# Kernel optimization log

Measured on AMD Instinct MI355X. Metric: run time of the kernel, lower is better.

The kernel has to match this reference:

```python
import jax, jax.numpy as jnp
import numpy as np

LN_EPS = 1e-5

def setup_inputs() -> dict:
    key = jax.random.key(0)
    ks = jax.random.split(key, 8)
    B, L, D, H = 4, 2048, 512, 8
    x = jax.random.normal(ks[0], (B, L, D), dtype=jnp.float32)
    token_ids = jax.random.randint(ks[1], (B, L), 0, 50000, dtype=jnp.int64)
    s = 1.0 / np.sqrt(D)
    Wq = jax.random.normal(ks[2], (D, D), dtype=jnp.float32) * s
    Wk = jax.random.normal(ks[3], (D, D), dtype=jnp.float32) * s
    Wv = jax.random.normal(ks[4], (D, D), dtype=jnp.float32) * s
    Wo = jax.random.normal(ks[5], (D, D), dtype=jnp.float32) * s
    gamma = jnp.ones((D,), dtype=jnp.float32)
    beta = jnp.zeros((D,), dtype=jnp.float32)
    return {"x": x, "token_ids": token_ids, "Wq": Wq, "Wk": Wk,
            "Wv": Wv, "Wo": Wo, "gamma": gamma, "beta": beta}

def reference(x, token_ids, Wq, Wk, Wv, Wo, gamma, beta):
    B, L, D = x.shape
    H = 8
    Dh = D // H
    residual = x
    # Pre-LN
    mu = jnp.mean(x, axis=-1, keepdims=True)
    var = jnp.mean(jnp.square(x - mu), axis=-1, keepdims=True)
    xn = (x - mu) * jax.lax.rsqrt(var + LN_EPS) * gamma + beta
    # projections (torch Linear: y = x @ W.T), split heads -> [B,H,L,Dh]
    def proj(W):
        return jnp.einsum('bld,ed->ble', xn, W).reshape(B, L, H, Dh).transpose(0, 2, 1, 3)
    Q, K, V = proj(Wq), proj(Wk), proj(Wv)
    scale = jnp.sqrt(jnp.float32(Dh))
    scores = jnp.einsum('bhqd,bhkd->bhqk', Q, K) / scale  # [B,H,L,L]
    neg_inf = jnp.float32(-jnp.inf)
    causal = jnp.triu(jnp.ones((L, L), dtype=bool), k=1)           # [L,L]
    pad = (token_ids == 0)[:, None, None, :]                       # [B,1,1,L]
    scores = jnp.where(causal[None, None], neg_inf, scores)
    scores = jnp.where(pad, neg_inf, scores)
    all_masked = jnp.all(jnp.isinf(scores), axis=-1, keepdims=True)
    scores = jnp.where(all_masked, 0.0, scores)
    attn = jax.nn.softmax(scores, axis=-1)  # dropout is identity in eval
    out = jnp.einsum('bhqk,bhkd->bhqd', attn, V)
    out = out.transpose(0, 2, 1, 3).reshape(B, L, D)
    out = jnp.einsum('bld,ed->ble', out, Wo)
    return residual + out
```

## Files before the change

kernel.cpp:

```cpp
#include <hip/hip_runtime.h>
#include <math.h>

typedef unsigned short u16;
typedef unsigned int u32;
typedef unsigned long long u64;
typedef float f32x4 __attribute__((ext_vector_type(4)));
typedef __bf16 bf16x8 __attribute__((ext_vector_type(8)));
typedef __bf16 bf16x4 __attribute__((ext_vector_type(4)));

constexpr int Bc = 4, Lc = 2048, Dc = 512, Hc = 8, DHc = 64;
constexpr int NTOK = Bc * Lc;
constexpr float LN_EPS = 1e-5f;
constexpr int PS = 72;
constexpr float QSCALE = 0.125f * 1.44269504088896340736f;
constexpr float MNEG = -1e30f;

__device__ inline u16 bf_bits(float f) {
  return __builtin_bit_cast(u16, (__bf16)f);
}

__global__ __launch_bounds__(256) void prep2_kernel(const float* __restrict__ s0,
                                                    const float* __restrict__ s1,
                                                    const float* __restrict__ s2,
                                                    const float* __restrict__ s3,
                                                    u16* __restrict__ d0,
                                                    u16* __restrict__ d1,
                                                    u16* __restrict__ d2,
                                                    u16* __restrict__ d3,
                                                    const int* __restrict__ tok,
                                                    u64* __restrict__ pm,
                                                    float* __restrict__ vm,
                                                    const float* __restrict__ x,
                                                    const float* __restrict__ gamma,
                                                    const float* __restrict__ beta,
                                                    u16* __restrict__ xn) {
  int bid = blockIdx.x;
  if (bid < 1024) {
    int mat = bid >> 8;
    int i = ((bid & 255) * 256 + threadIdx.x) * 4;
    const float* s = (mat == 0) ? s0 : (mat == 1) ? s1 : (mat == 2) ? s2 : s3;
    u16* d = (mat == 0) ? d0 : (mat == 1) ? d1 : (mat == 2) ? d2 : d3;
    float4 v = *(const float4*)&s[i];
    bf16x4 o;
    o[0] = (__bf16)v.x; o[1] = (__bf16)v.y; o[2] = (__bf16)v.z; o[3] = (__bf16)v.w;
    *(bf16x4*)&d[i] = o;
  } else if (bid < 1056) {
    int wid = ((bid - 1024) * 256 + threadIdx.x) >> 6;
    int lane = threadIdx.x & 63;
    u64 m = __ballot(tok[(size_t)wid * 64 + lane] == 0);
    if (lane == 0) pm[wid] = m;
    if (bid == 1024) {
      float4 z = make_float4(0.f, 0.f, 0.f, 0.f);
      *(float4*)&vm[threadIdx.x * 8] = z;
      *(float4*)&vm[threadIdx.x * 8 + 4] = z;
    }
  } else {
    int wave = threadIdx.x >> 6;
    int lane = threadIdx.x & 63;
    int row  = (bid - 1056) * 4 + wave;
    const float* xr = x + (size_t)row * Dc;
    float4 v0 = ((const float4*)xr)[lane * 2];
    float4 v1 = ((const float4*)xr)[lane * 2 + 1];
    float sum = v0.x + v0.y + v0.z + v0.w + v1.x + v1.y + v1.z + v1.w;
    float sq  = v0.x*v0.x + v0.y*v0.y + v0.z*v0.z + v0.w*v0.w
              + v1.x*v1.x + v1.y*v1.y + v1.z*v1.z + v1.w*v1.w;
    #pragma unroll
    for (int off = 32; off > 0; off >>= 1) {
      sum += __shfl_xor(sum, off);
      sq  += __shfl_xor(sq, off);
    }
    float mu = sum * (1.0f / Dc);
    float rs = rsqrtf(sq * (1.0f / Dc) - mu * mu + LN_EPS);
    float4 g0 = ((const float4*)gamma)[lane * 2];
    float4 g1 = ((const float4*)gamma)[lane * 2 + 1];
    float4 b0 = ((const float4*)beta)[lane * 2];
    float4 b1 = ((const float4*)beta)[lane * 2 + 1];
    bf16x8 o;
    o[0] = (__bf16)((v0.x - mu) * rs * g0.x + b0.x);
    o[1] = (__bf16)((v0.y - mu) * rs * g0.y + b0.y);
    o[2] = (__bf16)((v0.z - mu) * rs * g0.z + b0.z);
    o[3] = (__bf16)((v0.w - mu) * rs * g0.w + b0.w);
    o[4] = (__bf16)((v1.x - mu) * rs * g1.x + b1.x);
    o[5] = (__bf16)((v1.y - mu) * rs * g1.y + b1.y);
    o[6] = (__bf16)((v1.z - mu) * rs * g1.z + b1.z);
    o[7] = (__bf16)((v1.w - mu) * rs * g1.w + b1.w);
    *(bf16x8*)&xn[(size_t)row * Dc + lane * 8] = o;
  }
}

template <int MODE>
__global__ __launch_bounds__(256) void gemm_bf16(const u16* __restrict__ A,
                                                 const u16* __restrict__ W,
                                                 const float* __restrict__ res,
                                                 float* __restrict__ out_f,
                                                 u16* __restrict__ o_q,
                                                 u16* __restrict__ o_k,
                                                 u16* __restrict__ o_v,
                                                 float* __restrict__ vm) {
  __shared__ u16 As[2][128 * 64];
  __shared__ u16 Bs[2][128 * 64];
  int tid = threadIdx.x;
  int lane = tid & 63;
  int w = tid >> 6;
  int wr = w >> 1, wc = w & 1;
  int cc = lane & 15, rb = lane >> 4;
  int n0 = blockIdx.x * 128;
  int e0 = blockIdx.y * 128;

  auto stage = [&](int k0, int buf) {
    #pragma unroll
    for (int i = 0; i < 4; i++) {
      int s = (i * 4 + w) * 64 + lane;
      int row = s >> 3;
      int colp = (s & 7) ^ (row & 7);
      const char* gA = (const char*)&A[(size_t)(n0 + row) * Dc + k0] + colp * 16;
      const char* gB = (const char*)&W[(size_t)(e0 + row) * Dc + k0] + colp * 16;
      __builtin_amdgcn_global_load_lds(
          (const __attribute__((address_space(1))) void*)gA,
          (__attribute__((address_space(3))) void*)&As[buf][(i * 4 + w) * 512], 16, 0, 0);
      __builtin_amdgcn_global_load_lds(
          (const __attribute__((address_space(1))) void*)gB,
          (__attribute__((address_space(3))) void*)&Bs[buf][(i * 4 + w) * 512], 16, 0, 0);
    }
  };

  f32x4 acc[4][4] = {};
  stage(0, 0);
  for (int kt = 0; kt < 8; kt++) {
    int cur = kt & 1;
    if (kt < 7) {
      stage((kt + 1) << 6, cur ^ 1);
      asm volatile("s_waitcnt vmcnt(8)" ::: "memory");
    } else {
      asm volatile("s_waitcnt vmcnt(0)" ::: "memory");
    }
    __builtin_amdgcn_sched_barrier(0);
    __builtin_amdgcn_s_barrier();
    __builtin_amdgcn_sched_barrier(0);
    #pragma unroll
    for (int kk = 0; kk < 2; kk++) {
      bf16x8 aF[4], bF[4];
      #pragma unroll
      for (int m = 0; m < 4; m++) {
        int row = wr * 64 + m * 16 + cc;
        int cp = ((rb + kk * 4) ^ (cc & 7)) << 3;
        aF[m] = *(bf16x8*)&As[cur][row * 64 + cp];
      }
      #pragma unroll
      for (int n = 0; n < 4; n++) {
        int row = wc * 64 + n * 16 + cc;
        int cp = ((rb + kk * 4) ^ (cc & 7)) << 3;
        bF[n] = *(bf16x8*)&Bs[cur][row * 64 + cp];
      }
      #pragma unroll
      for (int m = 0; m < 4; m++)
        #pragma unroll
        for (int n = 0; n < 4; n++)
          acc[m][n] = __builtin_amdgcn_mfma_f32_16x16x32_bf16(aF[m], bF[n], acc[m][n], 0, 0, 0);
    }
    __syncthreads();
  }

  if (MODE == 3) {
    int bb = n0 >> 11;
    int mat = e0 >> 9;
    int e0c = e0 & 511;
    if (mat == 2) {
      #pragma unroll
      for (int n = 0; n < 4; n++) {
        int c = e0c + wc * 64 + n * 16 + cc;
        int h = c >> 6, dh = c & 63;
        float cp = 0.f;
        #pragma unroll
        for (int m = 0; m < 4; m++) {
          int l = (n0 + wr * 64 + m * 16 + rb * 4) & (Lc - 1);
          bf16x4 o4;
          o4[0] = (__bf16)acc[m][n][0]; o4[1] = (__bf16)acc[m][n][1];
          o4[2] = (__bf16)acc[m][n][2]; o4[3] = (__bf16)acc[m][n][3];
          size_t addr = ((((size_t)(bb * Hc + h)) * (Lc / 64) + (l >> 6)) * DHc + dh) * 64 + (l & 63);
          *(bf16x4*)&o_v[addr] = o4;
          cp += (acc[m][n][0] + acc[m][n][1]) + (acc[m][n][2] + acc[m][n][3]);
        }
        cp += __shfl_xor(cp, 16);
        cp += __shfl_xor(cp, 32);
        if (lane < 16) atomicAdd(&vm[(bb * Hc + h) * DHc + dh], cp);
      }
    } else {
      float sc = (mat == 0) ? QSCALE : 1.0f;
      u16* dst = (mat == 0) ? o_q : o_k;
      #pragma unroll
      for (int m = 0; m < 4; m++) {
        #pragma unroll
        for (int n = 0; n < 4; n++) {
          #pragma unroll
          for (int j = 0; j < 4; j++) {
            int r = n0 + wr * 64 + m * 16 + rb * 4 + j;
            int c = e0c + wc * 64 + n * 16 + cc;
            int ll = r & (Lc - 1);
            dst[(((size_t)(bb * Hc + (c >> 6))) * Lc + ll) * DHc + (c & 63)] = bf_bits(acc[m][n][j] * sc);
          }
        }
      }
    }
  } else {
    #pragma unroll
    for (int m = 0; m < 4; m++) {
      #pragma unroll
      for (int n = 0; n < 4; n++) {
        #pragma unroll
        for (int j = 0; j < 4; j++) {
          int r = n0 + wr * 64 + m * 16 + rb * 4 + j;
          int c = e0 + wc * 64 + n * 16 + cc;
          size_t o = (size_t)r * Dc + c;
          out_f[o] = acc[m][n][j] + res[o];
        }
      }
    }
  }
}

__global__ __launch_bounds__(64) void attn11(const u16* __restrict__ Q,
                                             const u16* __restrict__ K,
                                             const u16* __restrict__ VT,
                                             const float* __restrict__ vm,
                                             const u64* __restrict__ pmask,
                                             u16* __restrict__ out) {
  __shared__ u16 Ps[32 * PS];
  int lane = threadIdx.x;
  int cc = lane & 15, rb = lane >> 4;
  int bh = blockIdx.x;
  int qt = (int)gridDim.y - 1 - (int)blockIdx.y;
  int q0 = qt * 32;
  int b = bh >> 3, h = bh & 7;
  const u16* Qb = Q + (size_t)bh * Lc * DHc;
  const u16* Kb = K + (size_t)bh * Lc * DHc;
  const u16* Vb = VT + (size_t)bh * Lc * DHc;
  const u64* pmb = pmask + (b << 5);
  int nfull = q0 >> 6;

  bf16x8 qF[2][2];
  #pragma unroll
  for (int qb = 0; qb < 2; qb++)
    #pragma unroll
    for (int kc = 0; kc < 2; kc++)
      qF[qb][kc] = *(const bf16x8*)&Qb[(size_t)(q0 + qb * 16 + cc) * DHc + kc * 32 + rb * 8];

  float mrow[2] = {MNEG, MNEG};
  float lrow[2] = {0.f, 0.f};
  f32x4 acc[2][4] = {};

  bf16x8 kfA[4][2], kfB[4][2];
  {
    const u16* kp = Kb;
    #pragma unroll
    for (int c = 0; c < 4; c++) {
      kfA[c][0] = *(const bf16x8*)&kp[(c * 16 + cc) * DHc + rb * 8];
      kfA[c][1] = *(const bf16x8*)&kp[(c * 16 + cc) * DHc + 32 + rb * 8];
    }
  }
  if (nfull >= 1) {
    const u16* kp = Kb + (size_t)64 * DHc;
    #pragma unroll
    for (int c = 0; c < 4; c++) {
      kfB[c][0] = *(const bf16x8*)&kp[(c * 16 + cc) * DHc + rb * 8];
      kfB[c][1] = *(const bf16x8*)&kp[(c * 16 + cc) * DHc + 32 + rb * 8];
    }
  }

  auto body = [&](int kt, bf16x8 (&kf)[4][2]) {
    int k0 = kt * 64;
    bool last = (kt == nfull);
    u64 pm = pmb[kt];
    const u16* vp = Vb + (size_t)kt * (DHc * 64);
    bf16x8 vf[2][4];
    #pragma unroll
    for (int kc = 0; kc < 2; kc++)
      #pragma unroll
      for (int d0 = 0; d0 < 4; d0++)
        vf[kc][d0] = *(const bf16x8*)&vp[(d0 * 16 + cc) * 64 + kc * 32 + rb * 8];

    f32x4 sq[2][4] = {};
    __builtin_amdgcn_s_setprio(1);
    #pragma unroll
    for (int c = 0; c < 4; c++) {
      #pragma unroll
      for (int qb = 0; qb < 2; qb++) {
        sq[qb][c] = __builtin_amdgcn_mfma_f32_16x16x32_bf16(kf[c][0], qF[qb][0], sq[qb][c], 0, 0, 0);
        sq[qb][c] = __builtin_amdgcn_mfma_f32_16x16x32_bf16(kf[c][1], qF[qb][1], sq[qb][c], 0, 0, 0);
      }
    }
    __builtin_amdgcn_s_setprio(0);
    if (kt + 2 <= nfull) {
      const u16* kp = Kb + (size_t)(k0 + 128) * DHc;
      #pragma unroll
      for (int c = 0; c < 4; c++) {
        kf[c][0] = *(const bf16x8*)&kp[(c * 16 + cc) * DHc + rb * 8];
        kf[c][1] = *(const bf16x8*)&kp[(c * 16 + cc) * DHc + 32 + rb * 8];
      }
    }
    if (pm) {
      #pragma unroll
      for (int c = 0; c < 4; c++) {
        u32 smr = (((u32)(pm >> (c * 16)) & 0xffffu) >> (rb * 4));
        #pragma unroll
        for (int qb = 0; qb < 2; qb++)
          #pragma unroll
          for (int j = 0; j < 4; j++)
            if ((smr >> j) & 1) sq[qb][c][j] = -INFINITY;
      }
    }
    if (last) {
      #pragma unroll
      for (int qb = 0; qb < 2; qb++) {
        int qrel = q0 + qb * 16 + cc - k0;
        #pragma unroll
        for (int c = 0; c < 4; c++)
          #pragma unroll
          for (int j = 0; j < 4; j++)
            if (c * 16 + rb * 4 + j > qrel) sq[qb][c][j] = -INFINITY;
      }
    }
    #pragma unroll
    for (int qb = 0; qb < 2; qb++) {
      float m0 = fmaxf(fmaxf(sq[qb][0][0], sq[qb][0][1]), fmaxf(sq[qb][0][2], sq[qb][0][3]));
      float m1 = fmaxf(fmaxf(sq[qb][1][0], sq[qb][1][1]), fmaxf(sq[qb][1][2], sq[qb][1][3]));
      float m2 = fmaxf(fmaxf(sq[qb][2][0], sq[qb][2][1]), fmaxf(sq[qb][2][2], sq[qb][2][3]));
      float m3 = fmaxf(fmaxf(sq[qb][3][0], sq[qb][3][1]), fmaxf(sq[qb][3][2], sq[qb][3][3]));
      float mx = fmaxf(fmaxf(m0, m1), fmaxf(m2, m3));
      mx = fmaxf(mx, __shfl_xor(mx, 16));
      mx = fmaxf(mx, __shfl_xor(mx, 32));
      if (!__all(mx <= mrow[qb] + 8.f)) {
        float nm = fmaxf(mrow[qb], mx);
        float alpha = exp2f(mrow[qb] - nm);
        lrow[qb] *= alpha;
        #pragma unroll
        for (int d0 = 0; d0 < 4; d0++)
          #pragma unroll
          for (int j = 0; j < 4; j++)
            acc[qb][d0][j] *= alpha;
        mrow[qb] = nm;
      }
      float rs = 0.f;
      #pragma unroll
      for (int c = 0; c < 4; c++) {
        f32x4 p;
        #pragma unroll
        for (int j = 0; j < 4; j++) p[j] = exp2f(sq[qb][c][j] - mrow[qb]);
        rs += (p[0] + p[1]) + (p[2] + p[3]);
        bf16x4 p4;
        p4[0] = (__bf16)p[0]; p4[1] = (__bf16)p[1];
        p4[2] = (__bf16)p[2]; p4[3] = (__bf16)p[3];
        *(bf16x4*)&Ps[(qb * 16 + cc) * PS + c * 16 + rb * 4] = p4;
      }
      rs += __shfl_xor(rs, 16);
      rs += __shfl_xor(rs, 32);
      lrow[qb] += rs;
    }
    asm volatile("s_waitcnt lgkmcnt(0)" ::: "memory");
    __builtin_amdgcn_sched_barrier(0);
    __builtin_amdgcn_s_setprio(1);
    #pragma unroll
    for (int kc = 0; kc < 2; kc++) {
      bf16x8 pF0 = *(bf16x8*)&Ps[(size_t)cc * PS + kc * 32 + rb * 8];
      bf16x8 pF1 = *(bf16x8*)&Ps[(size_t)(16 + cc) * PS + kc * 32 + rb * 8];
      #pragma unroll
      for (int d0 = 0; d0 < 4; d0++) {
        acc[0][d0] = __builtin_amdgcn_mfma_f32_16x16x32_bf16(vf[kc][d0], pF0, acc[0][d0], 0, 0, 0);
        acc[1][d0] = __builtin_amdgcn_mfma_f32_16x16x32_bf16(vf[kc][d0], pF1, acc[1][d0], 0, 0, 0);
      }
    }
    __builtin_amdgcn_s_setprio(0);
  };

  for (int kt = 0; kt <= nfull; kt += 2) {
    body(kt, kfA);
    if (kt + 1 <= nfull) body(kt + 1, kfB);
  }

  #pragma unroll
  for (int qb = 0; qb < 2; qb++) {
    int q = q0 + qb * 16 + cc;
    bool ok = lrow[qb] > 0.f;
    float inv = ok ? 1.0f / lrow[qb] : 0.f;
    #pragma unroll
    for (int d0 = 0; d0 < 4; d0++) {
      bf16x4 o4;
      #pragma unroll
      for (int j = 0; j < 4; j++) {
        float v = ok ? acc[qb][d0][j] * inv
                     : vm[bh * DHc + d0 * 16 + rb * 4 + j] * (1.0f / Lc);
        o4[j] = (__bf16)v;
      }
      *(bf16x4*)&out[((size_t)(b * Lc + q)) * Dc + h * DHc + d0 * 16 + rb * 4] = o4;
    }
  }
}

extern "C" void kernel_launch(void* const* d_in, const int* in_sizes, int n_in,
                              void* d_out, int out_size, void* d_ws, size_t ws_size,
                              hipStream_t stream) {
  const float* x     = (const float*)d_in[0];
  const int*   tok   = (const int*)d_in[1];
  const float* Wq    = (const float*)d_in[2];
  const float* Wk    = (const float*)d_in[3];
  const float* Wv    = (const float*)d_in[4];
  const float* Wo    = (const float*)d_in[5];
  const float* gamma = (const float*)d_in[6];
  const float* beta  = (const float*)d_in[7];
  float* out = (float*)d_out;

  const size_t SEG = (size_t)NTOK * Dc;
  const size_t WSEG = (size_t)Dc * Dc;
  u16* xn   = (u16*)d_ws;
  u16* Qd   = xn + SEG;
  u16* Kd   = Qd + SEG;
  u16* VT   = Kd + SEG;
  u16* ao   = VT + SEG;
  u16* Wqkv = ao + SEG;
  u16* Wob  = Wqkv + 3 * WSEG;
  float* vm = (float*)(Wob + WSEG);
  u64* pmarr = (u64*)(vm + (size_t)Bc * Hc * DHc);

  prep2_kernel<<<3104, 256, 0, stream>>>(Wq, Wk, Wv, Wo,
                                         Wqkv, Wqkv + WSEG, Wqkv + 2 * WSEG, Wob,
                                         tok, pmarr, vm, x, gamma, beta, xn);

  dim3 gq(NTOK / 128, (3 * Dc) / 128);
  gemm_bf16<3><<<gq, 256, 0, stream>>>(xn, Wqkv, nullptr, nullptr, Qd, Kd, VT, vm);

  dim3 ga(Bc * Hc, Lc / 32);
  attn11<<<ga, 64, 0, stream>>>(Qd, Kd, VT, vm, pmarr, ao);

  dim3 gg(NTOK / 128, Dc / 128);
  gemm_bf16<0><<<gg, 256, 0, stream>>>(ao, Wob, x, out, nullptr, nullptr, nullptr, nullptr);
}
```

Measured before the change: 106.5 us.

## Rewrite attention with 32x32x16 MFMA and register-resident P via lane shuffles

The attention kernel now uses 32x32x16 bf16 MFMA tiles, with one 32-query row per lane pair, in place of 16x16x32 tiles. The softmax probabilities are packed to bf16 and exchanged across half-waves with shuffles to form the PV operand directly, so the LDS round trip for P is gone. The K double-buffer prefetch is dropped, and K is now loaded each iteration right before use. Output is staged through LDS so each lane writes 16-byte stores. This risks exposed K load latency, and the shuffle-based P layout is intricate to get right.

```diff
diff --git a/kernel.cpp b/kernel.cpp
--- a/kernel.cpp
+++ b/kernel.cpp
@@ -5,8 +5,11 @@
 typedef unsigned int u32;
 typedef unsigned long long u64;
 typedef float f32x4 __attribute__((ext_vector_type(4)));
+typedef float f32x16 __attribute__((ext_vector_type(16)));
 typedef __bf16 bf16x8 __attribute__((ext_vector_type(8)));
 typedef __bf16 bf16x4 __attribute__((ext_vector_type(4)));
+typedef __bf16 bf16x2 __attribute__((ext_vector_type(2)));
+typedef u32 u32x4 __attribute__((ext_vector_type(4)));
 
 constexpr int Bc = 4, Lc = 2048, Dc = 512, Hc = 8, DHc = 64;
 constexpr int NTOK = Bc * Lc;
@@ -17,6 +20,10 @@
 
 __device__ inline u16 bf_bits(float f) {
   return __builtin_bit_cast(u16, (__bf16)f);
+}
+__device__ inline u32 pk2(float a, float b) {
+  bf16x2 t; t[0] = (__bf16)a; t[1] = (__bf16)b;
+  return __builtin_bit_cast(u32, t);
 }
 
 __global__ __launch_bounds__(256) void prep2_kernel(const float* __restrict__ s0,
@@ -219,7 +226,7 @@
   }
 }
 
-__global__ __launch_bounds__(64) void attn11(const u16* __restrict__ Q,
+__global__ __launch_bounds__(64) void attn12(const u16* __restrict__ Q,
                                              const u16* __restrict__ K,
                                              const u16* __restrict__ VT,
                                              const float* __restrict__ vm,
@@ -227,7 +234,8 @@
                                              u16* __restrict__ out) {
   __shared__ u16 Ps[32 * PS];
   int lane = threadIdx.x;
-  int cc = lane & 15, rb = lane >> 4;
+  int ql = lane & 31;
+  int hi = lane >> 5;
   int bh = blockIdx.x;
   int qt = (int)gridDim.y - 1 - (int)blockIdx.y;
   int q0 = qt * 32;
@@ -238,160 +246,156 @@
   const u64* pmb = pmask + (b << 5);
   int nfull = q0 >> 6;
 
-  bf16x8 qF[2][2];
+  bf16x8 qF[4];
   #pragma unroll
-  for (int qb = 0; qb < 2; qb++)
-    #pragma unroll
-    for (int kc = 0; kc < 2; kc++)
-      qF[qb][kc] = *(const bf16x8*)&Qb[(size_t)(q0 + qb * 16 + cc) * DHc + kc * 32 + rb * 8];
-
-  float mrow[2] = {MNEG, MNEG};
-  float lrow[2] = {0.f, 0.f};
-  f32x4 acc[2][4] = {};
-
-  bf16x8 kfA[4][2], kfB[4][2];
-  {
-    const u16* kp = Kb;
-    #pragma unroll
-    for (int c = 0; c < 4; c++) {
-      kfA[c][0] = *(const bf16x8*)&kp[(c * 16 + cc) * DHc + rb * 8];
-      kfA[c][1] = *(const bf16x8*)&kp[(c * 16 + cc) * DHc + 32 + rb * 8];
-    }
-  }
-  if (nfull >= 1) {
-    const u16* kp = Kb + (size_t)64 * DHc;
-    #pragma unroll
-    for (int c = 0; c < 4; c++) {
-      kfB[c][0] = *(const bf16x8*)&kp[(c * 16 + cc) * DHc + rb * 8];
-      kfB[c][1] = *(const bf16x8*)&kp[(c * 16 + cc) * DHc + 32 + rb * 8];
-    }
-  }
-
-  auto body = [&](int kt, bf16x8 (&kf)[4][2]) {
+  for (int ds = 0; ds < 4; ds++)
+    qF[ds] = *(const bf16x8*)&Qb[(size_t)(q0 + ql) * DHc + ds * 16 + hi * 8];
+
+  float mrow = MNEG;
+  float lrow = 0.f;
+  f32x16 oacc0 = {}, oacc1 = {};
+
+  for (int kt = 0; kt <= nfull; kt++) {
     int k0 = kt * 64;
     bool last = (kt == nfull);
     u64 pm = pmb[kt];
+    f32x16 sq0 = {}, sq1 = {};
+    {
+      bf16x8 kf0[4], kf1[4];
+      #pragma unroll
+      for (int ds = 0; ds < 4; ds++) {
+        kf0[ds] = *(const bf16x8*)&Kb[(size_t)(k0 + ql) * DHc + ds * 16 + hi * 8];
+        kf1[ds] = *(const bf16x8*)&Kb[(size_t)(k0 + 32 + ql) * DHc + ds * 16 + hi * 8];
+      }
+      __builtin_amdgcn_s_setprio(1);
+      #pragma unroll
+      for (int ds = 0; ds < 4; ds++) {
+        sq0 = __builtin_amdgcn_mfma_f32_32x32x16_bf16(kf0[ds], qF[ds], sq0, 0, 0, 0);
+        sq1 = __builtin_amdgcn_mfma_f32_32x32x16_bf16(kf1[ds], qF[ds], sq1, 0, 0, 0);
+      }
+      __builtin_amdgcn_s_setprio(0);
+    }
+    __builtin_amdgcn_sched_barrier(0);
     const u16* vp = Vb + (size_t)kt * (DHc * 64);
-    bf16x8 vf[2][4];
-    #pragma unroll
-    for (int kc = 0; kc < 2; kc++)
-      #pragma unroll
-      for (int d0 = 0; d0 < 4; d0++)
-        vf[kc][d0] = *(const bf16x8*)&vp[(d0 * 16 + cc) * 64 + kc * 32 + rb * 8];
-
-    f32x4 sq[2][4] = {};
+    bf16x8 vf0[4], vf1[4];
+    #pragma unroll
+    for (int ks = 0; ks < 4; ks++) {
+      vf0[ks] = *(const bf16x8*)&vp[(size_t)ql * 64 + ks * 16 + hi * 8];
+      vf1[ks] = *(const bf16x8*)&vp[(size_t)(32 + ql) * 64 + ks * 16 + hi * 8];
+    }
+    if (pm) {
+      u64 pmh = pm >> (4 * hi);
+      #pragma unroll
+      for (int r = 0; r < 16; r++) {
+        int krb = (r & 3) + 8 * (r >> 2);
+        if ((pmh >> krb) & 1)        sq0[r] = -INFINITY;
+        if ((pmh >> (32 + krb)) & 1) sq1[r] = -INFINITY;
+      }
+    }
+    if (last) {
+      int qrel = q0 + ql - k0;
+      #pragma unroll
+      for (int r = 0; r < 16; r++) {
+        int krb = (r & 3) + 8 * (r >> 2) + 4 * hi;
+        if (krb > qrel)      sq0[r] = -INFINITY;
+        if (krb + 32 > qrel) sq1[r] = -INFINITY;
+      }
+    }
+    {
+      float mx = sq0[0];
+      #pragma unroll
+      for (int r = 1; r < 16; r++) mx = fmaxf(mx, sq0[r]);
+      #pragma unroll
+      for (int r = 0; r < 16; r++) mx = fmaxf(mx, sq1[r]);
+      if (!__all(mx <= mrow + 8.f)) {
+        float mf = fmaxf(mx, __shfl_xor(mx, 32));
+        float nm = fmaxf(mrow, mf);
+        float alpha = exp2f(mrow - nm);
+        lrow *= alpha;
+        #pragma unroll
+        for (int r = 0; r < 16; r++) { oacc0[r] *= alpha; oacc1[r] *= alpha; }
+        mrow = nm;
+      }
+      float rs = 0.f;
+      #pragma unroll
+      for (int r = 0; r < 16; r++) {
+        sq0[r] = exp2f(sq0[r] - mrow); rs += sq0[r];
+        sq1[r] = exp2f(sq1[r] - mrow); rs += sq1[r];
+      }
+      lrow += rs;
+    }
     __builtin_amdgcn_s_setprio(1);
     #pragma unroll
-    for (int c = 0; c < 4; c++) {
-      #pragma unroll
-      for (int qb = 0; qb < 2; qb++) {
-        sq[qb][c] = __builtin_amdgcn_mfma_f32_16x16x32_bf16(kf[c][0], qF[qb][0], sq[qb][c], 0, 0, 0);
-        sq[qb][c] = __builtin_amdgcn_mfma_f32_16x16x32_bf16(kf[c][1], qF[qb][1], sq[qb][c], 0, 0, 0);
+    for (int ks = 0; ks < 4; ks++) {
+      u32 u, v;
+      if (ks == 0)      { u = pk2(sq0[0], sq0[1]);  v = pk2(sq0[2], sq0[3]); }
+      else if (ks == 1) { u = pk2(sq0[8], sq0[9]);  v = pk2(sq0[10], sq0[11]); }
+      else if (ks == 2) { u = pk2(sq1[0], sq1[1]);  v = pk2(sq1[2], sq1[3]); }
+      else              { u = pk2(sq1[8], sq1[9]);  v = pk2(sq1[10], sq1[11]); }
+      u32 us = (u32)__shfl_xor((int)u, 32);
+      u32 vs = (u32)__shfl_xor((int)v, 32);
+      u32x4 wv;
+      wv[0] = hi ? us : u;
+      wv[1] = hi ? vs : v;
+      wv[2] = hi ? u : us;
+      wv[3] = hi ? v : vs;
+      f32x16 dummy = {};
+      (void)dummy; (void)wv;
+      u32 uB, vB;
+      if (ks == 0)      { uB = pk2(sq0[4], sq0[5]);  vB = pk2(sq0[6], sq0[7]); }
+      else if (ks == 1) { uB = pk2(sq0[12], sq0[13]); vB = pk2(sq0[14], sq0[15]); }
+      else if (ks == 2) { uB = pk2(sq1[4], sq1[5]);  vB = pk2(sq1[6], sq1[7]); }
+      else              { uB = pk2(sq1[12], sq1[13]); vB = pk2(sq1[14], sq1[15]); }
+      u32 usB = (u32)__shfl_xor((int)uB, 32);
+      u32 vsB = (u32)__shfl_xor((int)vB, 32);
+      u32x4 wf;
+      if (hi == 0) {
+        wf[0] = u;   wf[1] = v;
+        wf[2] = us;  wf[3] = vs;
+      } else {
+        wf[0] = usB; wf[1] = vsB;
+        wf[2] = uB;  wf[3] = vB;
+      }
+      bf16x8 pB = __builtin_bit_cast(bf16x8, wf);
+      if (ks < 2) {
+        oacc0 = __builtin_amdgcn_mfma_f32_32x32x16_bf16(vf0[ks], pB, oacc0, 0, 0, 0);
+        oacc1 = __builtin_amdgcn_mfma_f32_32x32x16_bf16(vf1[ks], pB, oacc1, 0, 0, 0);
+      } else {
+        oacc0 = __builtin_amdgcn_mfma_f32_32x32x16_bf16(vf0[ks], pB, oacc0, 0, 0, 0);
+        oacc1 = __builtin_amdgcn_mfma_f32_32x32x16_bf16(vf1[ks], pB, oacc1, 0, 0, 0);
       }
     }
     __builtin_amdgcn_s_setprio(0);
-    if (kt + 2 <= nfull) {
-      const u16* kp = Kb + (size_t)(k0 + 128) * DHc;
-      #pragma unroll
-      for (int c = 0; c < 4; c++) {
-        kf[c][0] = *(const bf16x8*)&kp[(c * 16 + cc) * DHc + rb * 8];
-        kf[c][1] = *(const bf16x8*)&kp[(c * 16 + cc) * DHc + 32 + rb * 8];
-      }
-    }
-    if (pm) {
-      #pragma unroll
-      for (int c = 0; c < 4; c++) {
-        u32 smr = (((u32)(pm >> (c * 16)) & 0xffffu) >> (rb * 4));
-        #pragma unroll
-        for (int qb = 0; qb < 2; qb++)
-          #pragma unroll
-          for (int j = 0; j < 4; j++)
-            if ((smr >> j) & 1) sq[qb][c][j] = -INFINITY;
-      }
-    }
-    if (last) {
-      #pragma unroll
-      for (int qb = 0; qb < 2; qb++) {
-        int qrel = q0 + qb * 16 + cc - k0;
-        #pragma unroll
-        for (int c = 0; c < 4; c++)
-          #pragma unroll
-          for (int j = 0; j < 4; j++)
-            if (c * 16 + rb * 4 + j > qrel) sq[qb][c][j] = -INFINITY;
-      }
-    }
-    #pragma unroll
-    for (int qb = 0; qb < 2; qb++) {
-      float m0 = fmaxf(fmaxf(sq[qb][0][0], sq[qb][0][1]), fmaxf(sq[qb][0][2], sq[qb][0][3]));
-      float m1 = fmaxf(fmaxf(sq[qb][1][0], sq[qb][1][1]), fmaxf(sq[qb][1][2], sq[qb][1][3]));
-      float m2 = fmaxf(fmaxf(sq[qb][2][0], sq[qb][2][1]), fmaxf(sq[qb][2][2], sq[qb][2][3]));
-      float m3 = fmaxf(fmaxf(sq[qb][3][0], sq[qb][3][1]), fmaxf(sq[qb][3][2], sq[qb][3][3]));
-      float mx = fmaxf(fmaxf(m0, m1), fmaxf(m2, m3));
-      mx = fmaxf(mx, __shfl_xor(mx, 16));
-      mx = fmaxf(mx, __shfl_xor(mx, 32));
-      if (!__all(mx <= mrow[qb] + 8.f)) {
-        float nm = fmaxf(mrow[qb], mx);
-        float alpha = exp2f(mrow[qb] - nm);
-        lrow[qb] *= alpha;
-        #pragma unroll
-        for (int d0 = 0; d0 < 4; d0++)
-          #pragma unroll
-          for (int j = 0; j < 4; j++)
-            acc[qb][d0][j] *= alpha;
-        mrow[qb] = nm;
-      }
-      float rs = 0.f;
-      #pragma unroll
-      for (int c = 0; c < 4; c++) {
-        f32x4 p;
-        #pragma unroll
-        for (int j = 0; j < 4; j++) p[j] = exp2f(sq[qb][c][j] - mrow[qb]);
-        rs += (p[0] + p[1]) + (p[2] + p[3]);
-        bf16x4 p4;
-        p4[0] = (__bf16)p[0]; p4[1] = (__bf16)p[1];
-        p4[2] = (__bf16)p[2]; p4[3] = (__bf16)p[3];
-        *(bf16x4*)&Ps[(qb * 16 + cc) * PS + c * 16 + rb * 4] = p4;
-      }
-      rs += __shfl_xor(rs, 16);
-      rs += __shfl_xor(rs, 32);
-      lrow[qb] += rs;
-    }
-    asm volatile("s_waitcnt lgkmcnt(0)" ::: "memory");
-    __builtin_amdgcn_sched_barrier(0);
-    __builtin_amdgcn_s_setprio(1);
-    #pragma unroll
-    for (int kc = 0; kc < 2; kc++) {
-      bf16x8 pF0 = *(bf16x8*)&Ps[(size_t)cc * PS + kc * 32 + rb * 8];
-      bf16x8 pF1 = *(bf16x8*)&Ps[(size_t)(16 + cc) * PS + kc * 32 + rb * 8];
-      #pragma unroll
-      for (int d0 = 0; d0 < 4; d0++) {
-        acc[0][d0] = __builtin_amdgcn_mfma_f32_16x16x32_bf16(vf[kc][d0], pF0, acc[0][d0], 0, 0, 0);
-        acc[1][d0] = __builtin_amdgcn_mfma_f32_16x16x32_bf16(vf[kc][d0], pF1, acc[1][d0], 0, 0, 0);
-      }
-    }
-    __builtin_amdgcn_s_setprio(0);
-  };
-
-  for (int kt = 0; kt <= nfull; kt += 2) {
-    body(kt, kfA);
-    if (kt + 1 <= nfull) body(kt + 1, kfB);
-  }
-
+  }
+
+  lrow += __shfl_xor(lrow, 32);
+
+  bool ok = lrow > 0.f;
+  float inv = ok ? 1.0f / lrow : 0.f;
   #pragma unroll
-  for (int qb = 0; qb < 2; qb++) {
-    int q = q0 + qb * 16 + cc;
-    bool ok = lrow[qb] > 0.f;
-    float inv = ok ? 1.0f / lrow[qb] : 0.f;
-    #pragma unroll
-    for (int d0 = 0; d0 < 4; d0++) {
-      bf16x4 o4;
-      #pragma unroll
-      for (int j = 0; j < 4; j++) {
-        float v = ok ? acc[qb][d0][j] * inv
-                     : vm[bh * DHc + d0 * 16 + rb * 4 + j] * (1.0f / Lc);
-        o4[j] = (__bf16)v;
-      }
-      *(bf16x4*)&out[((size_t)(b * Lc + q)) * Dc + h * DHc + d0 * 16 + rb * 4] = o4;
+  for (int rq = 0; rq < 4; rq++) {
+    #pragma unroll
+    for (int dblk = 0; dblk < 2; dblk++) {
+      int d = dblk * 32 + rq * 8 + 4 * hi;
+      float a0, a1, a2, a3;
+      if (dblk == 0) { a0 = oacc0[rq*4]; a1 = oacc0[rq*4+1]; a2 = oacc0[rq*4+2]; a3 = oacc0[rq*4+3]; }
+      else           { a0 = oacc1[rq*4]; a1 = oacc1[rq*4+1]; a2 = oacc1[rq*4+2]; a3 = oacc1[rq*4+3]; }
+      float v0 = ok ? a0 * inv : vm[bh * DHc + d] * (1.0f / Lc);
+      float v1 = ok ? a1 * inv : vm[bh * DHc + d + 1] * (1.0f / Lc);
+      float v2 = ok ? a2 * inv : vm[bh * DHc + d + 2] * (1.0f / Lc);
+      float v3 = ok ? a3 * inv : vm[bh * DHc + d + 3] * (1.0f / Lc);
+      *(u32*)&Ps[ql * PS + d]     = pk2(v0, v1);
+      *(u32*)&Ps[ql * PS + d + 2] = pk2(v2, v3);
+    }
+  }
+  asm volatile("s_waitcnt lgkmcnt(0)" ::: "memory");
+  __builtin_amdgcn_sched_barrier(0);
+  {
+    u16* dst = out + ((size_t)(b * Lc + q0 + ql)) * Dc + h * DHc + hi * 32;
+    #pragma unroll
+    for (int uq = 0; uq < 4; uq++) {
+      bf16x8 t = *(bf16x8*)&Ps[ql * PS + hi * 32 + uq * 8];
+      *(bf16x8*)&dst[uq * 8] = t;
     }
   }
 }
@@ -429,7 +433,7 @@
   gemm_bf16<3><<<gq, 256, 0, stream>>>(xn, Wqkv, nullptr, nullptr, Qd, Kd, VT, vm);
 
   dim3 ga(Bc * Hc, Lc / 32);
-  attn11<<<ga, 64, 0, stream>>>(Qd, Kd, VT, vm, pmarr, ao);
+  attn12<<<ga, 64, 0, stream>>>(Qd, Kd, VT, vm, pmarr, ao);
 
   dim3 gg(NTOK / 128, Dc / 128);
   gemm_bf16<0><<<gg, 256, 0, stream>>>(ao, Wob, x, out, nullptr, nullptr, nullptr, nullptr);
```

After: 117.1 us. +9.9%, slower.

## Software-pipeline QK^T MFMAs one tile ahead of softmax and PV in attention

Applied to the files above, without the earlier changes.

Splits the attention loop body into separate K-load, QK^T MFMA and softmax/PV stages. The QK^T for the next key tile is now issued before the softmax and PV work of the current tile, so matrix-core work can overlap the scalar softmax. The cost is a second set of score accumulators (sqA/sqB), which raises VGPR pressure in a one-wave block and may reduce occupancy.

```diff
diff --git a/kernel.cpp b/kernel.cpp
--- a/kernel.cpp
+++ b/kernel.cpp
@@ -219,7 +219,7 @@
   }
 }
 
-__global__ __launch_bounds__(64) void attn11(const u16* __restrict__ Q,
+__global__ __launch_bounds__(64) void attn13(const u16* __restrict__ Q,
                                              const u16* __restrict__ K,
                                              const u16* __restrict__ VT,
                                              const float* __restrict__ vm,
@@ -250,24 +250,34 @@
   f32x4 acc[2][4] = {};
 
   bf16x8 kfA[4][2], kfB[4][2];
-  {
-    const u16* kp = Kb;
+  f32x4 sqA[2][4], sqB[2][4];
+
+  auto loadK = [&](int kt, bf16x8 (&kf)[4][2]) {
+    const u16* kp = Kb + (size_t)(kt * 64) * DHc;
     #pragma unroll
     for (int c = 0; c < 4; c++) {
-      kfA[c][0] = *(const bf16x8*)&kp[(c * 16 + cc) * DHc + rb * 8];
-      kfA[c][1] = *(const bf16x8*)&kp[(c * 16 + cc) * DHc + 32 + rb * 8];
-    }
-  }
-  if (nfull >= 1) {
-    const u16* kp = Kb + (size_t)64 * DHc;
+      kf[c][0] = *(const bf16x8*)&kp[(c * 16 + cc) * DHc + rb * 8];
+      kf[c][1] = *(const bf16x8*)&kp[(c * 16 + cc) * DHc + 32 + rb * 8];
+    }
+  };
+  auto qkt = [&](bf16x8 (&kf)[4][2], f32x4 (&sq)[2][4]) {
+    #pragma unroll
+    for (int qb = 0; qb < 2; qb++)
+      #pragma unroll
+      for (int c = 0; c < 4; c++)
+        sq[qb][c] = f32x4{};
+    __builtin_amdgcn_s_setprio(1);
     #pragma unroll
     for (int c = 0; c < 4; c++) {
-      kfB[c][0] = *(const bf16x8*)&kp[(c * 16 + cc) * DHc + rb * 8];
-      kfB[c][1] = *(const bf16x8*)&kp[(c * 16 + cc) * DHc + 32 + rb * 8];
-    }
-  }
-
-  auto body = [&](int kt, bf16x8 (&kf)[4][2]) {
+      #pragma unroll
+      for (int qb = 0; qb < 2; qb++) {
+        sq[qb][c] = __builtin_amdgcn_mfma_f32_16x16x32_bf16(kf[c][0], qF[qb][0], sq[qb][c], 0, 0, 0);
+        sq[qb][c] = __builtin_amdgcn_mfma_f32_16x16x32_bf16(kf[c][1], qF[qb][1], sq[qb][c], 0, 0, 0);
+      }
+    }
+    __builtin_amdgcn_s_setprio(0);
+  };
+  auto process = [&](int kt, f32x4 (&sq)[2][4]) {
     int k0 = kt * 64;
     bool last = (kt == nfull);
     u64 pm = pmb[kt];
@@ -279,25 +289,6 @@
       for (int d0 = 0; d0 < 4; d0++)
         vf[kc][d0] = *(const bf16x8*)&vp[(d0 * 16 + cc) * 64 + kc * 32 + rb * 8];
 
-    f32x4 sq[2][4] = {};
-    __builtin_amdgcn_s_setprio(1);
-    #pragma unroll
-    for (int c = 0; c < 4; c++) {
-      #pragma unroll
-      for (int qb = 0; qb < 2; qb++) {
-        sq[qb][c] = __builtin_amdgcn_mfma_f32_16x16x32_bf16(kf[c][0], qF[qb][0], sq[qb][c], 0, 0, 0);
-        sq[qb][c] = __builtin_amdgcn_mfma_f32_16x16x32_bf16(kf[c][1], qF[qb][1], sq[qb][c], 0, 0, 0);
-      }
-    }
-    __builtin_amdgcn_s_setprio(0);
-    if (kt + 2 <= nfull) {
-      const u16* kp = Kb + (size_t)(k0 + 128) * DHc;
-      #pragma unroll
-      for (int c = 0; c < 4; c++) {
-        kf[c][0] = *(const bf16x8*)&kp[(c * 16 + cc) * DHc + rb * 8];
-        kf[c][1] = *(const bf16x8*)&kp[(c * 16 + cc) * DHc + 32 + rb * 8];
-      }
-    }
     if (pm) {
       #pragma unroll
       for (int c = 0; c < 4; c++) {
@@ -372,9 +363,18 @@
     __builtin_amdgcn_s_setprio(0);
   };
 
+  loadK(0, kfA);
+  qkt(kfA, sqA);
+  if (nfull >= 1) loadK(1, kfB);
   for (int kt = 0; kt <= nfull; kt += 2) {
-    body(kt, kfA);
-    if (kt + 1 <= nfull) body(kt + 1, kfB);
+    if (kt + 1 <= nfull) qkt(kfB, sqB);
+    if (kt + 2 <= nfull) loadK(kt + 2, kfA);
+    process(kt, sqA);
+    if (kt + 1 <= nfull) {
+      if (kt + 2 <= nfull) qkt(kfA, sqA);
+      if (kt + 3 <= nfull) loadK(kt + 3, kfB);
+      process(kt + 1, sqB);
+    }
   }
 
   #pragma unroll
@@ -429,7 +429,7 @@
   gemm_bf16<3><<<gq, 256, 0, stream>>>(xn, Wqkv, nullptr, nullptr, Qd, Kd, VT, vm);
 
   dim3 ga(Bc * Hc, Lc / 32);
-  attn11<<<ga, 64, 0, stream>>>(Qd, Kd, VT, vm, pmarr, ao);
+  attn13<<<ga, 64, 0, stream>>>(Qd, Kd, VT, vm, pmarr, ao);
 
   dim3 gg(NTOK / 128, Dc / 128);
   gemm_bf16<0><<<gg, 256, 0, stream>>>(ao, Wob, x, out, nullptr, nullptr, nullptr, nullptr);
```

After: 106.5 us. Within noise of the previous version (-0.0%).
